# Kernel tuning notes

Measured on AMD Instinct MI355X. Metric: run time of the kernel, lower is better.

The kernel has to match this reference:

```python
import jax, jax.numpy as jnp
import numpy as np

B, L, IN_DIM, OUT_DIM = 4, 2048, 64, 2
D_MODEL, N_LAYERS = 768, 4
D_STATE, EXPAND, D_CONV = 16, 2, 4
D_INNER = EXPAND * D_MODEL          # 1536
DT_RANK = -(-D_MODEL // 16)          # ceil(768/16) = 48
EPS = 1e-5


def rmsnorm(x, w):
    return x * jax.lax.rsqrt(jnp.mean(x * x, axis=-1, keepdims=True) + EPS) * w


def setup_inputs() -> dict:
    key = jax.random.key(0)
    ks = jax.random.split(key, 10)
    s = 0.02
    f = lambda k, shp: jax.random.normal(k, shp, jnp.float32) * s
    return dict(
        x=jax.random.normal(ks[0], (B, L, IN_DIM), jnp.float32),
        W1=f(ks[1], (D_MODEL, IN_DIM)),
        b1=jnp.zeros((D_MODEL,), jnp.float32),
        norm_w=jnp.ones((N_LAYERS, D_MODEL), jnp.float32),
        in_proj_w=f(ks[2], (N_LAYERS, 2 * D_INNER, D_MODEL)),
        conv_w=f(ks[3], (N_LAYERS, D_INNER, D_CONV)),
        conv_b=jnp.zeros((N_LAYERS, D_INNER), jnp.float32),
        x_proj_w=f(ks[4], (N_LAYERS, DT_RANK + 2 * D_STATE, D_INNER)),
        dt_proj_w=f(ks[5], (N_LAYERS, D_INNER, DT_RANK)),
        dt_proj_b=f(ks[6], (N_LAYERS, D_INNER)),
        A_log=jnp.log(jnp.broadcast_to(jnp.arange(1, D_STATE + 1, dtype=jnp.float32), (N_LAYERS, D_INNER, D_STATE))).copy(),
        D=jnp.ones((N_LAYERS, D_INNER), jnp.float32),
        out_proj_w=f(ks[7], (N_LAYERS, D_MODEL, D_INNER)),
        normf_w=jnp.ones((D_MODEL,), jnp.float32),
        W2=f(ks[8], (OUT_DIM, D_MODEL)),
        b2=jnp.zeros((OUT_DIM,), jnp.float32),
    )


def _block(h, p):
    # One Mamba residual block (mamba-minimal): h + out_proj(ssm(conv(in_proj(norm(h)))))
    norm_w, in_w, cw, cb, xp_w, dt_w, dt_b, A_log, Dp, out_w = p
    xn = rmsnorm(h, norm_w)
    xr = xn @ in_w.T                                  # [B,L,2*d_inner]
    xs, res = jnp.split(xr, 2, axis=-1)
    # causal depthwise conv1d, kernel D_CONV, left pad D_CONV-1
    xc = jax.lax.conv_general_dilated(
        xs.transpose(0, 2, 1), cw[:, None, :], (1,), [(D_CONV - 1, 0)],
        feature_group_count=D_INNER, dimension_numbers=('NCH', 'OIH', 'NCH'))
    xc = jax.nn.silu((xc + cb[None, :, None]).transpose(0, 2, 1))  # [B,L,d_inner]
    # selective SSM
    A = -jnp.exp(A_log)                               # [d_inner, n]
    dbl = xc @ xp_w.T                                 # [B,L,dt_rank+2n]
    dr = dbl[..., :DT_RANK]
    Bm = dbl[..., DT_RANK:DT_RANK + D_STATE]          # [B,L,n]
    Cm = dbl[..., DT_RANK + D_STATE:]                 # [B,L,n]
    delta = jax.nn.softplus(dr @ dt_w.T + dt_b)       # [B,L,d_inner]

    def step(s, t):
        d_t, B_t, C_t, u_t = t                        # [B,d_in],[B,n],[B,n],[B,d_in]
        dA = jnp.exp(d_t[..., None] * A)              # [B,d_in,n]
        s = dA * s + (d_t * u_t)[..., None] * B_t[:, None, :]
        y = jnp.einsum('bdn,bn->bd', s, C_t)
        return s, y

    init = jnp.zeros((h.shape[0], D_INNER, D_STATE), h.dtype)
    ts = (delta.transpose(1, 0, 2), Bm.transpose(1, 0, 2),
          Cm.transpose(1, 0, 2), xc.transpose(1, 0, 2))
    _, ys = jax.lax.scan(step, init, ts)
    y = ys.transpose(1, 0, 2) + xc * Dp               # [B,L,d_inner]
    y = y * jax.nn.silu(res)
    return h + y @ out_w.T


def _forward(x, W1, b1, norm_w, in_proj_w, conv_w, conv_b, x_proj_w,
             dt_proj_w, dt_proj_b, A_log, D, out_proj_w, normf_w, W2, b2):
    h = x @ W1.T + b1                                 # [B,L,d_model]
    params = (norm_w, in_proj_w, conv_w, conv_b, x_proj_w, dt_proj_w,
              dt_proj_b, A_log, D, out_proj_w)
    h, _ = jax.lax.scan(lambda c, p: (_block(c, p), None), h, params)
    h = rmsnorm(h, normf_w)
    logits = h @ W2.T + b2                            # [B,L,out_dim]
    probs = jax.nn.softmax(logits, axis=1)            # Softmax(dim=1) over L
    return probs.reshape(-1)                          # x.flatten()


def reference(x, W1, b1, norm_w, in_proj_w, conv_w, conv_b, x_proj_w,
              dt_proj_w, dt_proj_b, A_log, D, out_proj_w, normf_w, W2, b2):
    return _forward(x, W1, b1, norm_w, in_proj_w, conv_w, conv_b, x_proj_w,
                    dt_proj_w, dt_proj_b, A_log, D, out_proj_w, normf_w, W2, b2)
```

## Files before the change

kernel.cpp:

```cpp
#include <hip/hip_runtime.h>

typedef __bf16 bf16_t;
typedef bf16_t bf16x8 __attribute__((ext_vector_type(8)));
typedef float f32x4 __attribute__((ext_vector_type(4)));

#define DEV_INLINE __device__ __forceinline__

#define BB 4
#define LL 2048
#define ROWS 8192
#define DMODEL 768
#define DINNER 1536
#define DIN2 3072
#define DTRANK 48
#define DSTATE 16

DEV_INLINE void glds16(const void* g, void* l) {
    __builtin_amdgcn_global_load_lds(
        (const __attribute__((address_space(1))) void*)(unsigned long long)g,
        (__attribute__((address_space(3))) void*)(unsigned int)(unsigned long long)l,
        16, 0, 0);
}

DEV_INLINE float bf2f(bf16_t v) { return (float)v; }
DEV_INLINE bf16_t f2bf(float v) { return (bf16_t)v; }

struct Ptrs { const void* p[16]; };

__device__ __constant__ const int g_off[16] = {
    0, 524288, 573440, 574208, 577280, 10014464, 10039040, 10045184,
    10536704, 10831616, 10837760, 10936064, 10942208, 15660800, 15661568, 15663104
};
__device__ __constant__ const int g_sz[16] = {
    524288, 49152, 768, 3072, 9437184, 24576, 6144, 491520,
    294912, 6144, 98304, 6144, 4718592, 768, 1536, 2
};
#define CONV_ELEMS 15663112

__global__ __launch_bounds__(256) void convert_inputs(Ptrs P, bf16_t* __restrict__ dst,
                                                      float* __restrict__ Aa)
{
    int i = blockIdx.x * 256 + threadIdx.x;
    if (i >= CONV_ELEMS) return;
    bool isbf = (*(const unsigned*)P.p[3] == 0x3F803F80u);
    int seg = -1; int rel = 0;
#pragma unroll
    for (int s = 0; s < 16; ++s) {
        int r = i - g_off[s];
        if (r >= 0 && r < g_sz[s]) { seg = s; rel = r; }
    }
    if (seg < 0) return;
    const void* sp = P.p[seg];
    float fv = isbf ? bf2f(((const bf16_t*)sp)[rel]) : ((const float*)sp)[rel];
    dst[i] = f2bf(fv);
    if (seg == 10) Aa[rel] = -__expf(fv);
}

__global__ __launch_bounds__(256) void gemm_bt128(
    const bf16_t* __restrict__ A, int lda,
    const bf16_t* __restrict__ W, int ldw,
    void* __restrict__ Cv, int ldc, int K,
    const bf16_t* __restrict__ bias, int epi)
{
    __shared__ bf16_t sA[128 * 64];
    __shared__ bf16_t sW[128 * 64];
    const int t = threadIdx.x;
    const int wv = t >> 6, lane = t & 63;
    const int qk = lane >> 4, lr = lane & 15;
    const int m0 = blockIdx.x * 128, n0 = blockIdx.y * 128;
    const int wm = (wv >> 1) * 64, wn = (wv & 1) * 64;

    f32x4 acc[4][4];
#pragma unroll
    for (int i = 0; i < 4; ++i)
#pragma unroll
        for (int j = 0; j < 4; ++j) acc[i][j] = (f32x4){0.f, 0.f, 0.f, 0.f};

    for (int k0 = 0; k0 < K; k0 += 64) {
        __syncthreads();
#pragma unroll
        for (int j = 0; j < 4; ++j) {
            int ci = (wv * 4 + j) * 64 + lane;
            int row = ci >> 3;
            int c = ci & 7;
            int g = c ^ (row & 7);
            const char* srcA = (const char*)(A + (size_t)(m0 + row) * lda + k0) + g * 16;
            const char* srcW = (const char*)(W + (size_t)(n0 + row) * ldw + k0) + g * 16;
            glds16(srcA, (char*)sA + ci * 16);
            glds16(srcW, (char*)sW + ci * 16);
        }
        __syncthreads();

#pragma unroll
        for (int h = 0; h < 2; ++h) {
            bf16x8 af[4], wf[4];
#pragma unroll
            for (int i = 0; i < 4; ++i) {
                int row = wm + i * 16 + lr;
                int cc = (h * 4 + qk) ^ (row & 7);
                af[i] = *(const bf16x8*)((const char*)sA + row * 128 + cc * 16);
            }
#pragma unroll
            for (int j = 0; j < 4; ++j) {
                int row = wn + j * 16 + lr;
                int cc = (h * 4 + qk) ^ (row & 7);
                wf[j] = *(const bf16x8*)((const char*)sW + row * 128 + cc * 16);
            }
#pragma unroll
            for (int i = 0; i < 4; ++i)
#pragma unroll
                for (int j = 0; j < 4; ++j)
                    acc[i][j] = __builtin_amdgcn_mfma_f32_16x16x32_bf16(af[i], wf[j], acc[i][j], 0, 0, 0);
        }
    }

    float* Cf = (float*)Cv;
    bf16_t* Cb = (bf16_t*)Cv;
#pragma unroll
    for (int i = 0; i < 4; ++i) {
        int row = m0 + wm + i * 16 + qk * 4;
#pragma unroll
        for (int j = 0; j < 4; ++j) {
            int col = n0 + wn + j * 16 + lr;
#pragma unroll
            for (int r = 0; r < 4; ++r) {
                size_t idx = (size_t)(row + r) * ldc + col;
                float v = acc[i][j][r];
                if (epi == 1) v += bf2f(bias[col]);
                if (epi == 2) v += Cf[idx];
                if (epi == 3) Cb[idx] = f2bf(v);
                else Cf[idx] = v;
            }
        }
    }
}

__global__ __launch_bounds__(256) void gemm_outproj(
    const bf16_t* __restrict__ A,
    const bf16_t* __restrict__ W,
    float* __restrict__ Cf)
{
    __shared__ bf16_t sA[64 * 64];
    __shared__ bf16_t sW[128 * 64];
    const int t = threadIdx.x;
    const int wv = t >> 6, lane = t & 63;
    const int qk = lane >> 4, lr = lane & 15;
    const int m0 = blockIdx.x * 64, n0 = blockIdx.y * 128;
    const int wm = (wv >> 1) * 32, wn = (wv & 1) * 64;

    f32x4 acc[2][4];
#pragma unroll
    for (int i = 0; i < 2; ++i)
#pragma unroll
        for (int j = 0; j < 4; ++j) acc[i][j] = (f32x4){0.f, 0.f, 0.f, 0.f};

    for (int k0 = 0; k0 < DINNER; k0 += 64) {
        __syncthreads();
#pragma unroll
        for (int j = 0; j < 2; ++j) {
            int ci = (wv * 2 + j) * 64 + lane;
            int row = ci >> 3;
            int g = (ci & 7) ^ (row & 7);
            const char* srcA = (const char*)(A + (size_t)(m0 + row) * DINNER + k0) + g * 16;
            glds16(srcA, (char*)sA + ci * 16);
        }
#pragma unroll
        for (int j = 0; j < 4; ++j) {
            int ci = (wv * 4 + j) * 64 + lane;
            int row = ci >> 3;
            int g = (ci & 7) ^ (row & 7);
            const char* srcW = (const char*)(W + (size_t)(n0 + row) * DINNER + k0) + g * 16;
            glds16(srcW, (char*)sW + ci * 16);
        }
        __syncthreads();

#pragma unroll
        for (int h = 0; h < 2; ++h) {
            bf16x8 af[2], wf[4];
#pragma unroll
            for (int i = 0; i < 2; ++i) {
                int row = wm + i * 16 + lr;
                int cc = (h * 4 + qk) ^ (row & 7);
                af[i] = *(const bf16x8*)((const char*)sA + row * 128 + cc * 16);
            }
#pragma unroll
            for (int j = 0; j < 4; ++j) {
                int row = wn + j * 16 + lr;
                int cc = (h * 4 + qk) ^ (row & 7);
                wf[j] = *(const bf16x8*)((const char*)sW + row * 128 + cc * 16);
            }
#pragma unroll
            for (int i = 0; i < 2; ++i)
#pragma unroll
                for (int j = 0; j < 4; ++j)
                    acc[i][j] = __builtin_amdgcn_mfma_f32_16x16x32_bf16(af[i], wf[j], acc[i][j], 0, 0, 0);
        }
    }

#pragma unroll
    for (int i = 0; i < 2; ++i) {
        int row = m0 + wm + i * 16 + qk * 4;
#pragma unroll
        for (int j = 0; j < 4; ++j) {
            int col = n0 + wn + j * 16 + lr;
#pragma unroll
            for (int r = 0; r < 4; ++r) {
                size_t idx = (size_t)(row + r) * DMODEL + col;
                Cf[idx] += acc[i][j][r];
            }
        }
    }
}

__global__ __launch_bounds__(256) void gemm_xproj(
    const bf16_t* __restrict__ A,
    const bf16_t* __restrict__ W,
    float* __restrict__ Cp)
{
    __shared__ bf16_t sA[64 * 32];
    __shared__ bf16_t sW[80 * 32];
    const int t = threadIdx.x;
    const int wv = t >> 6, lane = t & 63;
    const int qk = lane >> 4, lr = lane & 15;
    const int m0 = blockIdx.x * 64;
    const int z  = blockIdx.y;
    const int wm = wv * 16;

    f32x4 acc[5];
#pragma unroll
    for (int j = 0; j < 5; ++j) acc[j] = (f32x4){0.f, 0.f, 0.f, 0.f};

    const int kbeg = z * (DINNER / 2), kend = kbeg + DINNER / 2;
    for (int k0 = kbeg; k0 < kend; k0 += 32) {
        __syncthreads();
        {
            int chunk = wv * 64 + lane;
            int row = chunk >> 2;
            int c = chunk & 3;
            int g = c ^ ((row >> 1) & 3);
            const char* srcA = (const char*)(A + (size_t)(m0 + row) * DINNER + k0) + g * 16;
            glds16(srcA, (char*)sA + wv * 1024);
        }
        for (int issue = wv; issue < 5; issue += 4) {
            int chunk = issue * 64 + lane;
            int row = chunk >> 2;
            int c = chunk & 3;
            int g = c ^ ((row >> 1) & 3);
            const char* srcW = (const char*)(W + (size_t)row * DINNER + k0) + g * 16;
            glds16(srcW, (char*)sW + issue * 1024);
        }
        __syncthreads();

        int rowa = wm + lr;
        int cca = qk ^ ((rowa >> 1) & 3);
        bf16x8 af = *(const bf16x8*)((const char*)sA + rowa * 64 + cca * 16);
#pragma unroll
        for (int j = 0; j < 5; ++j) {
            int roww = j * 16 + lr;
            int ccw = qk ^ ((roww >> 1) & 3);
            bf16x8 wf = *(const bf16x8*)((const char*)sW + roww * 64 + ccw * 16);
            acc[j] = __builtin_amdgcn_mfma_f32_16x16x32_bf16(af, wf, acc[j], 0, 0, 0);
        }
    }

    float* Co = Cp + (size_t)z * ROWS * 80;
    int row = m0 + wm + qk * 4;
#pragma unroll
    for (int j = 0; j < 5; ++j) {
        int col = j * 16 + lr;
#pragma unroll
        for (int r = 0; r < 4; ++r)
            Co[(size_t)(row + r) * 80 + col] = acc[j][r];
    }
}

__global__ __launch_bounds__(256) void xproj_combine(
    const float* __restrict__ Cp, bf16_t* __restrict__ dbl)
{
    int i = blockIdx.x * 256 + threadIdx.x;
    if (i < ROWS * 80)
        dbl[i] = f2bf(Cp[i] + Cp[(size_t)ROWS * 80 + i]);
}

__global__ __launch_bounds__(256) void gemm_dtproj(
    const bf16_t* __restrict__ A,
    const bf16_t* __restrict__ W,
    const bf16_t* __restrict__ bias,
    bf16_t* __restrict__ C)
{
    __shared__ bf16_t sA[128 * 64];
    __shared__ bf16_t sW[128 * 64];
    const int t = threadIdx.x;
    const int wv = t >> 6, lane = t & 63;
    const int qk = lane >> 4, lr = lane & 15;
    const int m0 = blockIdx.x * 128, n0 = blockIdx.y * 128;
    const int wm = (wv >> 1) * 64, wn = (wv & 1) * 64;

#pragma unroll
    for (int j = 0; j < 4; ++j) {
        int ci = j * 256 + t;
        int row = ci >> 3;
        int g = (ci & 7) ^ (row & 7);
        int gb = g * 16;
        uint4 va = {0u, 0u, 0u, 0u}, vw = {0u, 0u, 0u, 0u};
        if (gb < 96) {
            va = *(const uint4*)((const char*)(A + (size_t)(m0 + row) * 80) + gb);
            vw = *(const uint4*)((const char*)(W + (size_t)(n0 + row) * DTRANK) + gb);
        }
        *(uint4*)((char*)sA + ci * 16) = va;
        *(uint4*)((char*)sW + ci * 16) = vw;
    }
    __syncthreads();

    f32x4 acc[4][4];
#pragma unroll
    for (int i = 0; i < 4; ++i)
#pragma unroll
        for (int j = 0; j < 4; ++j) acc[i][j] = (f32x4){0.f, 0.f, 0.f, 0.f};

#pragma unroll
    for (int h = 0; h < 2; ++h) {
        bf16x8 af[4], wf[4];
#pragma unroll
        for (int i = 0; i < 4; ++i) {
            int row = wm + i * 16 + lr;
            int cc = (h * 4 + qk) ^ (row & 7);
            af[i] = *(const bf16x8*)((const char*)sA + row * 128 + cc * 16);
        }
#pragma unroll
        for (int j = 0; j < 4; ++j) {
            int row = wn + j * 16 + lr;
            int cc = (h * 4 + qk) ^ (row & 7);
            wf[j] = *(const bf16x8*)((const char*)sW + row * 128 + cc * 16);
        }
#pragma unroll
        for (int i = 0; i < 4; ++i)
#pragma unroll
            for (int j = 0; j < 4; ++j)
                acc[i][j] = __builtin_amdgcn_mfma_f32_16x16x32_bf16(af[i], wf[j], acc[i][j], 0, 0, 0);
    }

#pragma unroll
    for (int i = 0; i < 4; ++i) {
        int row = m0 + wm + i * 16 + qk * 4;
#pragma unroll
        for (int j = 0; j < 4; ++j) {
            int col = n0 + wn + j * 16 + lr;
            float bv = bf2f(bias[col]);
#pragma unroll
            for (int r = 0; r < 4; ++r) {
                float v = acc[i][j][r] + bv;
                v = (v > 30.f) ? v : log1pf(__expf(v));
                C[(size_t)(row + r) * DINNER + col] = f2bf(v);
            }
        }
    }
}

__global__ __launch_bounds__(256) void rmsnorm_kernel(
    const float* __restrict__ h, const bf16_t* __restrict__ w, bf16_t* __restrict__ out)
{
    int row = blockIdx.x;
    int tid = threadIdx.x;
    const float* hr = h + (size_t)row * DMODEL;
    float ss = 0.f;
    for (int k = tid; k < DMODEL; k += 256) { float v = hr[k]; ss += v * v; }
#pragma unroll
    for (int off = 32; off > 0; off >>= 1) ss += __shfl_down(ss, off);
    __shared__ float red[4];
    if ((tid & 63) == 0) red[tid >> 6] = ss;
    __syncthreads();
    float tot = red[0] + red[1] + red[2] + red[3];
    float scale = rsqrtf(tot / (float)DMODEL + 1e-5f);
    for (int k = tid; k < DMODEL; k += 256)
        out[(size_t)row * DMODEL + k] = f2bf(hr[k] * scale * bf2f(w[k]));
}

__global__ __launch_bounds__(256) void conv_silu_kernel(
    const bf16_t* __restrict__ xr, const bf16_t* __restrict__ cw,
    const bf16_t* __restrict__ cb, bf16_t* __restrict__ xc)
{
    int idx = blockIdx.x * 256 + threadIdx.x;
    int row = idx / 192;
    int d8 = (idx - row * 192) * 8;
    int l = row & (LL - 1);

    bf16x8 cbv = *(const bf16x8*)(cb + d8);
    bf16x8 cw4[4];
#pragma unroll
    for (int m = 0; m < 4; ++m) cw4[m] = *(const bf16x8*)(cw + d8 * 4 + m * 8);

    float acc[8];
#pragma unroll
    for (int k = 0; k < 8; ++k) acc[k] = bf2f(cbv[k]);

#pragma unroll
    for (int j = 0; j < 4; ++j) {
        if (l - 3 + j >= 0) {
            bf16x8 xv = *(const bf16x8*)(xr + (size_t)(row - 3 + j) * DIN2 + d8);
#pragma unroll
            for (int k = 0; k < 8; ++k) {
                int wi = k * 4 + j;
                acc[k] += bf2f(xv[k]) * bf2f(cw4[wi >> 3][wi & 7]);
            }
        }
    }
    bf16x8 ov;
#pragma unroll
    for (int k = 0; k < 8; ++k) {
        float s = acc[k] / (1.f + __expf(-acc[k]));
        ov[k] = f2bf(s);
    }
    *(bf16x8*)(xc + (size_t)row * DINNER + d8) = ov;
}

__global__ __launch_bounds__(256) void scan_p1(
    const bf16_t* __restrict__ delta, const bf16_t* __restrict__ xc,
    const bf16_t* __restrict__ dbl, const float* __restrict__ Aa_l,
    float* __restrict__ carryDt, float* __restrict__ carryE,
    int nchunk, int clen)
{
    int d = blockIdx.x * 256 + threadIdx.x;
    int b = blockIdx.y / nchunk, c = blockIdx.y - b * nchunk;
    float Aa[DSTATE];
#pragma unroll
    for (int n = 0; n < DSTATE; ++n) Aa[n] = Aa_l[d * DSTATE + n];
    float Aa0 = Aa[0];
    bool geo = true;
#pragma unroll
    for (int n = 1; n < DSTATE; ++n)
        geo = geo && (fabsf(Aa[n] - (float)(n + 1) * Aa0) <= 0.02f * (float)(n + 1) * fabsf(Aa0));

    float s[DSTATE];
#pragma unroll
    for (int n = 0; n < DSTATE; ++n) s[n] = 0.f;
    float dtsum = 0.f;
    int row0 = b * LL + c * clen;

    if (geo) {
        for (int tt = 0; tt < clen; ++tt) {
            size_t row = row0 + tt;
            float dt = bf2f(delta[row * DINNER + d]);
            float du = dt * bf2f(xc[row * DINNER + d]);
            bf16x8 B0 = *(const bf16x8*)(dbl + row * 80 + 48);
            bf16x8 B1 = *(const bf16x8*)(dbl + row * 80 + 56);
            float r = __expf(dt * Aa0);
            float dA = 1.f;
#pragma unroll
            for (int n = 0; n < DSTATE; ++n) {
                float bv = (n < 8) ? bf2f(B0[n & 7]) : bf2f(B1[n & 7]);
                dA *= r;
                s[n] = dA * s[n] + du * bv;
            }
            dtsum += dt;
        }
    } else {
        for (int tt = 0; tt < clen; ++tt) {
            size_t row = row0 + tt;
            float dt = bf2f(delta[row * DINNER + d]);
            float du = dt * bf2f(xc[row * DINNER + d]);
            bf16x8 B0 = *(const bf16x8*)(dbl + row * 80 + 48);
            bf16x8 B1 = *(const bf16x8*)(dbl + row * 80 + 56);
#pragma unroll
            for (int n = 0; n < DSTATE; ++n) {
                float bv = (n < 8) ? bf2f(B0[n & 7]) : bf2f(B1[n & 7]);
                float dA = __expf(dt * Aa[n]);
                s[n] = dA * s[n] + du * bv;
            }
            dtsum += dt;
        }
    }

    size_t eb = ((size_t)(b * nchunk + c) * DINNER + d) * DSTATE;
#pragma unroll
    for (int n = 0; n < DSTATE; ++n) carryE[eb + n] = s[n];
    carryDt[(size_t)(b * nchunk + c) * DINNER + d] = dtsum;
}

__global__ __launch_bounds__(256) void scan_p2(
    const float* __restrict__ carryDt, float* __restrict__ carryE,
    const float* __restrict__ Aa_l, int nchunk)
{
    int idx = blockIdx.x * 256 + threadIdx.x;
    int n = idx & 15;
    int bd = idx >> 4;
    int b = bd / DINNER, d = bd - b * DINNER;
    float Aa = Aa_l[d * DSTATE + n];
    float act = 0.f;
    for (int c = 0; c < nchunk; ++c) {
        size_t rowbase = (size_t)(b * nchunk + c) * DINNER + d;
        float P = __expf(carryDt[rowbase] * Aa);
        size_t ep = rowbase * DSTATE + n;
        float E = carryE[ep];
        carryE[ep] = act;
        act = P * act + E;
    }
}

__global__ __launch_bounds__(256) void scan_p3(
    const bf16_t* __restrict__ delta, const bf16_t* __restrict__ xc,
    const bf16_t* __restrict__ dbl, const float* __restrict__ Aa_l,
    const float* __restrict__ carryInit, const bf16_t* __restrict__ xr,
    const bf16_t* __restrict__ Dp_l, bf16_t* __restrict__ y,
    int nchunk, int clen)
{
    int d = blockIdx.x * 256 + threadIdx.x;
    int b = blockIdx.y / nchunk, c = blockIdx.y - b * nchunk;
    float Aa[DSTATE];
#pragma unroll
    for (int n = 0; n < DSTATE; ++n) Aa[n] = Aa_l[d * DSTATE + n];
    float Aa0 = Aa[0];
    bool geo = true;
#pragma unroll
    for (int n = 1; n < DSTATE; ++n)
        geo = geo && (fabsf(Aa[n] - (float)(n + 1) * Aa0) <= 0.02f * (float)(n + 1) * fabsf(Aa0));

    float s[DSTATE];
    size_t eb = ((size_t)(b * nchunk + c) * DINNER + d) * DSTATE;
#pragma unroll
    for (int n = 0; n < DSTATE; ++n) s[n] = carryInit[eb + n];
    float Dv = bf2f(Dp_l[d]);
    int row0 = b * LL + c * clen;

    if (geo) {
        for (int tt = 0; tt < clen; ++tt) {
            size_t row = row0 + tt;
            float dt = bf2f(delta[row * DINNER + d]);
            float u = bf2f(xc[row * DINNER + d]);
            float du = dt * u;
            bf16x8 B0 = *(const bf16x8*)(dbl + row * 80 + 48);
            bf16x8 B1 = *(const bf16x8*)(dbl + row * 80 + 56);
            bf16x8 C0 = *(const bf16x8*)(dbl + row * 80 + 64);
            bf16x8 C1 = *(const bf16x8*)(dbl + row * 80 + 72);
            float r = __expf(dt * Aa0);
            float dA = 1.f;
            float yv = 0.f;
#pragma unroll
            for (int n = 0; n < DSTATE; ++n) {
                float bv = (n < 8) ? bf2f(B0[n & 7]) : bf2f(B1[n & 7]);
                float cvv = (n < 8) ? bf2f(C0[n & 7]) : bf2f(C1[n & 7]);
                dA *= r;
                s[n] = dA * s[n] + du * bv;
                yv += s[n] * cvv;
            }
            float res = bf2f(xr[row * DIN2 + DINNER + d]);
            float sr = res / (1.f + __expf(-res));
            y[row * DINNER + d] = f2bf((yv + u * Dv) * sr);
        }
    } else {
        for (int tt = 0; tt < clen; ++tt) {
            size_t row = row0 + tt;
            float dt = bf2f(delta[row * DINNER + d]);
            float u = bf2f(xc[row * DINNER + d]);
            float du = dt * u;
            bf16x8 B0 = *(const bf16x8*)(dbl + row * 80 + 48);
            bf16x8 B1 = *(const bf16x8*)(dbl + row * 80 + 56);
            bf16x8 C0 = *(const bf16x8*)(dbl + row * 80 + 64);
            bf16x8 C1 = *(const bf16x8*)(dbl + row * 80 + 72);
            float yv = 0.f;
#pragma unroll
            for (int n = 0; n < DSTATE; ++n) {
                float bv = (n < 8) ? bf2f(B0[n & 7]) : bf2f(B1[n & 7]);
                float cvv = (n < 8) ? bf2f(C0[n & 7]) : bf2f(C1[n & 7]);
                float dA = __expf(dt * Aa[n]);
                s[n] = dA * s[n] + du * bv;
                yv += s[n] * cvv;
            }
            float res = bf2f(xr[row * DIN2 + DINNER + d]);
            float sr = res / (1.f + __expf(-res));
            y[row * DINNER + d] = f2bf((yv + u * Dv) * sr);
        }
    }
}

__global__ __launch_bounds__(256) void head_kernel(
    const bf16_t* __restrict__ hn, const bf16_t* __restrict__ W2,
    const bf16_t* __restrict__ b2, float* __restrict__ logits)
{
    int wv = threadIdx.x >> 6, lane = threadIdx.x & 63;
    int row = blockIdx.x * 4 + wv;
    const bf16_t* hr = hn + (size_t)row * DMODEL;
    float a0 = 0.f, a1 = 0.f;
    for (int k = lane; k < DMODEL; k += 64) {
        float x = bf2f(hr[k]);
        a0 += x * bf2f(W2[k]);
        a1 += x * bf2f(W2[DMODEL + k]);
    }
#pragma unroll
    for (int off = 32; off > 0; off >>= 1) {
        a0 += __shfl_down(a0, off);
        a1 += __shfl_down(a1, off);
    }
    if (lane == 0) {
        logits[(size_t)row * 2 + 0] = a0 + bf2f(b2[0]);
        logits[(size_t)row * 2 + 1] = a1 + bf2f(b2[1]);
    }
}

__global__ __launch_bounds__(256) void softmax_kernel(
    const float* __restrict__ logits, void* __restrict__ outv,
    const void* __restrict__ norm_raw)
{
    bool isbf = (*(const unsigned*)norm_raw == 0x3F803F80u);
    int b = blockIdx.x >> 1, o = blockIdx.x & 1;
    int tid = threadIdx.x;
    __shared__ float red[256];
    float mx = -1e30f;
    for (int l = tid; l < LL; l += 256)
        mx = fmaxf(mx, logits[(size_t)(b * LL + l) * 2 + o]);
    red[tid] = mx; __syncthreads();
    for (int s2 = 128; s2 > 0; s2 >>= 1) {
        if (tid < s2) red[tid] = fmaxf(red[tid], red[tid + s2]);
        __syncthreads();
    }
    mx = red[0];
    __syncthreads();
    float sum = 0.f;
    for (int l = tid; l < LL; l += 256)
        sum += __expf(logits[(size_t)(b * LL + l) * 2 + o] - mx);
    red[tid] = sum; __syncthreads();
    for (int s2 = 128; s2 > 0; s2 >>= 1) {
        if (tid < s2) red[tid] += red[tid + s2];
        __syncthreads();
    }
    float inv = 1.f / red[0];
    for (int l = tid; l < LL; l += 256) {
        float e = __expf(logits[(size_t)(b * LL + l) * 2 + o] - mx);
        float p = e * inv;
        if (!(p == p)) p = 999.0f;
        size_t oi = (size_t)(b * LL + l) * 2 + o;
        if (isbf) ((bf16_t*)outv)[oi] = f2bf(p);
        else      ((float*)outv)[oi] = p;
    }
}

extern "C" void kernel_launch(void* const* d_in, const int* in_sizes, int n_in,
                              void* d_out, int out_size, void* d_ws, size_t ws_size,
                              hipStream_t stream)
{
    char* ws = (char*)d_ws;
    bf16_t* cv     = (bf16_t*)(ws + 0ull);
    float*  Aaf    = (float*) (ws + 31326464ull);
    float*  h      = (float*) (ws + 31719680ull);
    bf16_t* xr     = (bf16_t*)(ws + 56885504ull);
    bf16_t* xny    = (bf16_t*)(ws + 107217152ull);
    bf16_t* xc     = (bf16_t*)(ws + 132382976ull);
    bf16_t* delta  = (bf16_t*)(ws + 157548800ull);
    bf16_t* dbl    = (bf16_t*)(ws + 182714624ull);
    float*  logits = (float*) (ws + 184025344ull);
    const size_t fixed_end = 184090880ull;
    float* dblP = (float*)(ws + 157548800ull);

    int nchunk = 16;
    if (ws_size >= fixed_end + 417792ull * 64) nchunk = 64;
    else if (ws_size >= fixed_end + 417792ull * 32) nchunk = 32;
    int clen = LL / nchunk;
    float* carryE  = (float*)(ws + fixed_end);
    float* carryDt = (float*)(ws + fixed_end + 393216ull * nchunk);

    const bf16_t* x      = cv + 0;
    const bf16_t* W1     = cv + 524288;
    const bf16_t* b1     = cv + 573440;
    const bf16_t* norm_w = cv + 574208;
    const bf16_t* in_w   = cv + 577280;
    const bf16_t* conv_w = cv + 10014464;
    const bf16_t* conv_b = cv + 10039040;
    const bf16_t* xp_w   = cv + 10045184;
    const bf16_t* dt_w   = cv + 10536704;
    const bf16_t* dt_b   = cv + 10831616;
    const bf16_t* Dp     = cv + 10936064;
    const bf16_t* out_w  = cv + 10942208;
    const bf16_t* normf_w= cv + 15660800;
    const bf16_t* W2     = cv + 15661568;
    const bf16_t* b2     = cv + 15663104;

    dim3 blk(256);

    Ptrs P;
    for (int i = 0; i < 16; ++i) P.p[i] = d_in[i];
    convert_inputs<<<(CONV_ELEMS + 255) / 256, blk, 0, stream>>>(P, cv, Aaf);

    bf16_t* xn = xny;
    bf16_t* y  = xny;

    gemm_bt128<<<dim3(64, 6), blk, 0, stream>>>(x, 64, W1, 64, (void*)h, DMODEL, 64, b1, 1);

    for (int l = 0; l < 4; ++l) {
        const bf16_t* in_w_l  = in_w  + (size_t)l * DIN2 * DMODEL;
        const bf16_t* xp_w_l  = xp_w  + (size_t)l * 80 * DINNER;
        const bf16_t* dt_w_l  = dt_w  + (size_t)l * DINNER * DTRANK;
        const bf16_t* out_w_l = out_w + (size_t)l * DMODEL * DINNER;
        const float*  Aa_l    = Aaf   + (size_t)l * DINNER * DSTATE;

        rmsnorm_kernel<<<ROWS, blk, 0, stream>>>(h, norm_w + l * DMODEL, xn);
        gemm_bt128<<<dim3(64, 24), blk, 0, stream>>>(xn, DMODEL, in_w_l, DMODEL,
                                                     (void*)xr, DIN2, DMODEL, nullptr, 3);
        conv_silu_kernel<<<ROWS * 192 / 256, blk, 0, stream>>>(xr, conv_w + l * DINNER * 4,
                                                               conv_b + l * DINNER, xc);
        gemm_xproj<<<dim3(128, 2), blk, 0, stream>>>(xc, xp_w_l, dblP);
        xproj_combine<<<ROWS * 80 / 256, blk, 0, stream>>>(dblP, dbl);
        gemm_dtproj<<<dim3(64, 12), blk, 0, stream>>>(dbl, dt_w_l, dt_b + l * DINNER, delta);
        scan_p1<<<dim3(6, BB * nchunk), blk, 0, stream>>>(delta, xc, dbl, Aa_l,
                                                          carryDt, carryE, nchunk, clen);
        scan_p2<<<BB * DINNER * DSTATE / 256, blk, 0, stream>>>(carryDt, carryE, Aa_l, nchunk);
        scan_p3<<<dim3(6, BB * nchunk), blk, 0, stream>>>(delta, xc, dbl, Aa_l, carryE,
                                                          xr, Dp + l * DINNER, y, nchunk, clen);
        gemm_outproj<<<dim3(128, 6), blk, 0, stream>>>(y, out_w_l, h);
    }

    rmsnorm_kernel<<<ROWS, blk, 0, stream>>>(h, normf_w, xn);
    head_kernel<<<ROWS / 4, blk, 0, stream>>>(xn, W2, b2, logits);
    softmax_kernel<<<8, blk, 0, stream>>>(logits, (void*)d_out, d_in[3]);
}
```

Before: 1.296 ms.

## Double-buffer GEMM LDS tiles with K=32 stages and allow 128 scan chunks

Both the generic 128x128 GEMM and the out-projection GEMM now use two LDS buffers of K=32 slices. The next slice is prefetched with global_load_lds while MFMAs run on the current one, which removes one barrier per iteration and overlaps memory with compute. The XOR swizzle is adapted to the 64-byte row stride. The chunked scan may also use 128 chunks when the workspace is large enough, adding parallelism at the cost of more carry storage and carry fix-up work.

```diff
diff --git a/kernel.cpp b/kernel.cpp
--- a/kernel.cpp
+++ b/kernel.cpp
@@ -62,56 +62,70 @@
     void* __restrict__ Cv, int ldc, int K,
     const bf16_t* __restrict__ bias, int epi)
 {
-    __shared__ bf16_t sA[128 * 64];
-    __shared__ bf16_t sW[128 * 64];
+    __shared__ bf16_t sA[2][128 * 32];
+    __shared__ bf16_t sW[2][128 * 32];
     const int t = threadIdx.x;
     const int wv = t >> 6, lane = t & 63;
     const int qk = lane >> 4, lr = lane & 15;
     const int m0 = blockIdx.x * 128, n0 = blockIdx.y * 128;
     const int wm = (wv >> 1) * 64, wn = (wv & 1) * 64;
 
+    int ch0 = (wv * 2 + 0) * 64 + lane;
+    int ch1 = (wv * 2 + 1) * 64 + lane;
+    int r0 = ch0 >> 2, g0 = (ch0 & 3) ^ ((r0 >> 1) & 3);
+    int r1 = ch1 >> 2, g1 = (ch1 & 3) ^ ((r1 >> 1) & 3);
+
     f32x4 acc[4][4];
 #pragma unroll
     for (int i = 0; i < 4; ++i)
 #pragma unroll
         for (int j = 0; j < 4; ++j) acc[i][j] = (f32x4){0.f, 0.f, 0.f, 0.f};
 
-    for (int k0 = 0; k0 < K; k0 += 64) {
+    {
+        const char* a0 = (const char*)(A + (size_t)(m0 + r0) * lda) + g0 * 16;
+        const char* a1 = (const char*)(A + (size_t)(m0 + r1) * lda) + g1 * 16;
+        const char* w0 = (const char*)(W + (size_t)(n0 + r0) * ldw) + g0 * 16;
+        const char* w1 = (const char*)(W + (size_t)(n0 + r1) * ldw) + g1 * 16;
+        glds16(a0, (char*)sA[0] + ch0 * 16);
+        glds16(a1, (char*)sA[0] + ch1 * 16);
+        glds16(w0, (char*)sW[0] + ch0 * 16);
+        glds16(w1, (char*)sW[0] + ch1 * 16);
+    }
+
+    int nIter = K >> 5;
+    for (int it = 0; it < nIter; ++it) {
+        int cur = it & 1;
         __syncthreads();
+        if (it + 1 < nIter) {
+            int k1 = (it + 1) << 5;
+            const char* a0 = (const char*)(A + (size_t)(m0 + r0) * lda + k1) + g0 * 16;
+            const char* a1 = (const char*)(A + (size_t)(m0 + r1) * lda + k1) + g1 * 16;
+            const char* w0 = (const char*)(W + (size_t)(n0 + r0) * ldw + k1) + g0 * 16;
+            const char* w1 = (const char*)(W + (size_t)(n0 + r1) * ldw + k1) + g1 * 16;
+            glds16(a0, (char*)sA[1 - cur] + ch0 * 16);
+            glds16(a1, (char*)sA[1 - cur] + ch1 * 16);
+            glds16(w0, (char*)sW[1 - cur] + ch0 * 16);
+            glds16(w1, (char*)sW[1 - cur] + ch1 * 16);
+        }
+
+        bf16x8 af[4], wf[4];
+#pragma unroll
+        for (int i = 0; i < 4; ++i) {
+            int row = wm + i * 16 + lr;
+            int cc = qk ^ ((row >> 1) & 3);
+            af[i] = *(const bf16x8*)((const char*)sA[cur] + row * 64 + cc * 16);
+        }
 #pragma unroll
         for (int j = 0; j < 4; ++j) {
-            int ci = (wv * 4 + j) * 64 + lane;
-            int row = ci >> 3;
-            int c = ci & 7;
-            int g = c ^ (row & 7);
-            const char* srcA = (const char*)(A + (size_t)(m0 + row) * lda + k0) + g * 16;
-            const char* srcW = (const char*)(W + (size_t)(n0 + row) * ldw + k0) + g * 16;
-            glds16(srcA, (char*)sA + ci * 16);
-            glds16(srcW, (char*)sW + ci * 16);
-        }
-        __syncthreads();
-
-#pragma unroll
-        for (int h = 0; h < 2; ++h) {
-            bf16x8 af[4], wf[4];
-#pragma unroll
-            for (int i = 0; i < 4; ++i) {
-                int row = wm + i * 16 + lr;
-                int cc = (h * 4 + qk) ^ (row & 7);
-                af[i] = *(const bf16x8*)((const char*)sA + row * 128 + cc * 16);
-            }
-#pragma unroll
-            for (int j = 0; j < 4; ++j) {
-                int row = wn + j * 16 + lr;
-                int cc = (h * 4 + qk) ^ (row & 7);
-                wf[j] = *(const bf16x8*)((const char*)sW + row * 128 + cc * 16);
-            }
-#pragma unroll
-            for (int i = 0; i < 4; ++i)
-#pragma unroll
-                for (int j = 0; j < 4; ++j)
-                    acc[i][j] = __builtin_amdgcn_mfma_f32_16x16x32_bf16(af[i], wf[j], acc[i][j], 0, 0, 0);
-        }
+            int row = wn + j * 16 + lr;
+            int cc = qk ^ ((row >> 1) & 3);
+            wf[j] = *(const bf16x8*)((const char*)sW[cur] + row * 64 + cc * 16);
+        }
+#pragma unroll
+        for (int i = 0; i < 4; ++i)
+#pragma unroll
+            for (int j = 0; j < 4; ++j)
+                acc[i][j] = __builtin_amdgcn_mfma_f32_16x16x32_bf16(af[i], wf[j], acc[i][j], 0, 0, 0);
     }
 
     float* Cf = (float*)Cv;
@@ -140,61 +154,65 @@
     const bf16_t* __restrict__ W,
     float* __restrict__ Cf)
 {
-    __shared__ bf16_t sA[64 * 64];
-    __shared__ bf16_t sW[128 * 64];
+    __shared__ bf16_t sA[2][64 * 32];
+    __shared__ bf16_t sW[2][128 * 32];
     const int t = threadIdx.x;
     const int wv = t >> 6, lane = t & 63;
     const int qk = lane >> 4, lr = lane & 15;
     const int m0 = blockIdx.x * 64, n0 = blockIdx.y * 128;
     const int wm = (wv >> 1) * 32, wn = (wv & 1) * 64;
 
+    int ca = wv * 64 + lane;
+    int ra = ca >> 2, ga = (ca & 3) ^ ((ra >> 1) & 3);
+    int cw0 = (wv * 2 + 0) * 64 + lane;
+    int cw1 = (wv * 2 + 1) * 64 + lane;
+    int rw0 = cw0 >> 2, gw0 = (cw0 & 3) ^ ((rw0 >> 1) & 3);
+    int rw1 = cw1 >> 2, gw1 = (cw1 & 3) ^ ((rw1 >> 1) & 3);
+
     f32x4 acc[2][4];
 #pragma unroll
     for (int i = 0; i < 2; ++i)
 #pragma unroll
         for (int j = 0; j < 4; ++j) acc[i][j] = (f32x4){0.f, 0.f, 0.f, 0.f};
 
-    for (int k0 = 0; k0 < DINNER; k0 += 64) {
+    {
+        glds16((const char*)(A + (size_t)(m0 + ra) * DINNER) + ga * 16, (char*)sA[0] + ca * 16);
+        glds16((const char*)(W + (size_t)(n0 + rw0) * DINNER) + gw0 * 16, (char*)sW[0] + cw0 * 16);
+        glds16((const char*)(W + (size_t)(n0 + rw1) * DINNER) + gw1 * 16, (char*)sW[0] + cw1 * 16);
+    }
+
+    const int nIter = DINNER / 32;
+    for (int it = 0; it < nIter; ++it) {
+        int cur = it & 1;
         __syncthreads();
-#pragma unroll
-        for (int j = 0; j < 2; ++j) {
-            int ci = (wv * 2 + j) * 64 + lane;
-            int row = ci >> 3;
-            int g = (ci & 7) ^ (row & 7);
-            const char* srcA = (const char*)(A + (size_t)(m0 + row) * DINNER + k0) + g * 16;
-            glds16(srcA, (char*)sA + ci * 16);
+        if (it + 1 < nIter) {
+            int k1 = (it + 1) << 5;
+            glds16((const char*)(A + (size_t)(m0 + ra) * DINNER + k1) + ga * 16,
+                   (char*)sA[1 - cur] + ca * 16);
+            glds16((const char*)(W + (size_t)(n0 + rw0) * DINNER + k1) + gw0 * 16,
+                   (char*)sW[1 - cur] + cw0 * 16);
+            glds16((const char*)(W + (size_t)(n0 + rw1) * DINNER + k1) + gw1 * 16,
+                   (char*)sW[1 - cur] + cw1 * 16);
+        }
+
+        bf16x8 af[2], wf[4];
+#pragma unroll
+        for (int i = 0; i < 2; ++i) {
+            int row = wm + i * 16 + lr;
+            int cc = qk ^ ((row >> 1) & 3);
+            af[i] = *(const bf16x8*)((const char*)sA[cur] + row * 64 + cc * 16);
         }
 #pragma unroll
         for (int j = 0; j < 4; ++j) {
-            int ci = (wv * 4 + j) * 64 + lane;
-            int row = ci >> 3;
-            int g = (ci & 7) ^ (row & 7);
-            const char* srcW = (const char*)(W + (size_t)(n0 + row) * DINNER + k0) + g * 16;
-            glds16(srcW, (char*)sW + ci * 16);
-        }
-        __syncthreads();
-
-#pragma unroll
-        for (int h = 0; h < 2; ++h) {
-            bf16x8 af[2], wf[4];
-#pragma unroll
-            for (int i = 0; i < 2; ++i) {
-                int row = wm + i * 16 + lr;
-                int cc = (h * 4 + qk) ^ (row & 7);
-                af[i] = *(const bf16x8*)((const char*)sA + row * 128 + cc * 16);
-            }
-#pragma unroll
-            for (int j = 0; j < 4; ++j) {
-                int row = wn + j * 16 + lr;
-                int cc = (h * 4 + qk) ^ (row & 7);
-                wf[j] = *(const bf16x8*)((const char*)sW + row * 128 + cc * 16);
-            }
-#pragma unroll
-            for (int i = 0; i < 2; ++i)
-#pragma unroll
-                for (int j = 0; j < 4; ++j)
-                    acc[i][j] = __builtin_amdgcn_mfma_f32_16x16x32_bf16(af[i], wf[j], acc[i][j], 0, 0, 0);
-        }
+            int row = wn + j * 16 + lr;
+            int cc = qk ^ ((row >> 1) & 3);
+            wf[j] = *(const bf16x8*)((const char*)sW[cur] + row * 64 + cc * 16);
+        }
+#pragma unroll
+        for (int i = 0; i < 2; ++i)
+#pragma unroll
+            for (int j = 0; j < 4; ++j)
+                acc[i][j] = __builtin_amdgcn_mfma_f32_16x16x32_bf16(af[i], wf[j], acc[i][j], 0, 0, 0);
     }
 
 #pragma unroll
@@ -652,7 +670,8 @@
     float* dblP = (float*)(ws + 157548800ull);
 
     int nchunk = 16;
-    if (ws_size >= fixed_end + 417792ull * 64) nchunk = 64;
+    if (ws_size >= fixed_end + 417792ull * 128) nchunk = 128;
+    else if (ws_size >= fixed_end + 417792ull * 64) nchunk = 64;
     else if (ws_size >= fixed_end + 417792ull * 32) nchunk = 32;
     int clen = LL / nchunk;
     float* carryE  = (float*)(ws + fixed_end);
```

Result: slower. 1.387 ms (+7.0%).
